# Optimization experiments

Measured on AMD Instinct MI355X. Metric: run time of the kernel, lower is better.

The kernel has to match this reference:

```python
import jax, jax.numpy as jnp
import numpy as np

DIM = 1024
HEADS = 8
DIM_HEAD = 64
INNER = HEADS * DIM_HEAD  # 512


def setup_inputs() -> dict:
    key = jax.random.key(0)
    k1, k2, k3, k4 = jax.random.split(key, 4)
    x = jax.random.normal(k1, (4, 4096, DIM), dtype=jnp.float32)
    W_qkv = jax.random.normal(k2, (DIM, 3 * INNER), dtype=jnp.float32) * (DIM ** -0.5)
    W_out = jax.random.normal(k3, (INNER, DIM), dtype=jnp.float32) * (INNER ** -0.5)
    b_out = jax.random.normal(k4, (DIM,), dtype=jnp.float32) * 0.01
    return {"x": x, "W_qkv": W_qkv, "W_out": W_out, "b_out": b_out}


def reference(x, W_qkv, W_out, b_out):
    b, n, _ = x.shape
    qkv = x @ W_qkv                                   # [b, n, 3*inner]
    q, k, v = jnp.split(qkv, 3, axis=-1)              # each [b, n, inner]

    def to_heads(t):
        return t.reshape(b, n, HEADS, DIM_HEAD).transpose(0, 2, 1, 3)  # [b, h, n, d]

    q = jax.nn.elu(to_heads(q)) + 1.0
    k = jax.nn.elu(to_heads(k)) + 1.0
    v = to_heads(v)
    # kv summary matrix: [b, h, d, e]
    context = jnp.einsum('bhnd,bhne->bhde', k, v)
    out = jnp.einsum('bhde,bhnd->bhne', context, q)   # [b, h, n, e]
    out = out.transpose(0, 2, 1, 3).reshape(b, n, INNER)
    return out @ W_out + b_out
```

## Files before the change

kernel.cpp:

```cpp
#include <hip/hip_runtime.h>
#include <hip/hip_bf16.h>
#include <cstdint>

typedef __attribute__((ext_vector_type(4))) float f32x4;
typedef __attribute__((ext_vector_type(8))) short bf16x8;

__device__ __forceinline__ ushort f2bf(float f) {
  unsigned u = __builtin_bit_cast(unsigned, f);
  u += 0x7fffu + ((u >> 16) & 1u);
  return (ushort)(u >> 16);
}

__device__ __forceinline__ void gload_lds16(const ushort* g, ushort* l) {
  __builtin_amdgcn_global_load_lds(
      (const __attribute__((address_space(1))) unsigned int*)g,
      (__attribute__((address_space(3))) unsigned int*)l, 16, 0, 0);
}

__device__ __forceinline__ void hard_barrier() {
  __builtin_amdgcn_sched_barrier(0);
  __builtin_amdgcn_s_barrier();
  __builtin_amdgcn_sched_barrier(0);
}

template <int N>
__device__ __forceinline__ void wait_vm() {
  if constexpr (N == 0) asm volatile("s_waitcnt vmcnt(0)" ::: "memory");
  else if constexpr (N == 2) asm volatile("s_waitcnt vmcnt(2)" ::: "memory");
  else if constexpr (N == 3) asm volatile("s_waitcnt vmcnt(3)" ::: "memory");
  else if constexpr (N == 4) asm volatile("s_waitcnt vmcnt(4)" ::: "memory");
  else static_assert(N < 0, "unsupported vmcnt");
}

__device__ __forceinline__ float elu1(float v) {
  return (v > 0.f) ? (v + 1.f) : __expf(v);
}

__global__ __launch_bounds__(256) void prep_kernel(const float4* __restrict__ x,
                                                   ushort4* __restrict__ xb,
                                                   const float* __restrict__ W,
                                                   ushort* __restrict__ Wt) {
  if (blockIdx.x < 2048) {
    const int n4 = 16384 * 1024 / 4;
    const int stride = 2048 * 256;
    for (int i = blockIdx.x * 256 + threadIdx.x; i < n4; i += stride) {
      float4 f = x[i];
      ushort4 o;
      o.x = f2bf(f.x); o.y = f2bf(f.y); o.z = f2bf(f.z); o.w = f2bf(f.w);
      xb[i] = o;
    }
  } else {
    __shared__ float tile[32][33];
    const int tb = blockIdx.x - 2048;
    const int n0 = (tb % 48) * 32;
    const int k0 = (tb / 48) * 32;
    const int tx = threadIdx.x & 31;
    const int ty = threadIdx.x >> 5;
    #pragma unroll
    for (int p = 0; p < 4; ++p) {
      int k = k0 + ty + p * 8;
      tile[ty + p * 8][tx] = W[(size_t)k * 1536 + n0 + tx];
    }
    __syncthreads();
    #pragma unroll
    for (int p = 0; p < 4; ++p) {
      int n = n0 + ty + p * 8;
      Wt[(size_t)n * 1024 + k0 + tx] = f2bf(tile[tx][ty + p * 8]);
    }
  }
}

template <int LDA, int LDB, int NT>
__device__ __forceinline__ void gemm_core32(const ushort* __restrict__ A,
                                            const ushort* __restrict__ Bt,
                                            int row0, int col0, f32x4 acc[4][4],
                                            ushort* lds) {
  const int tid = threadIdx.x;
  const int l = tid & 63;
  const int wid = tid >> 6;
  const int fr = l & 15;
  const int fq = l >> 4;
  const int wr = wid >> 2;
  const int wc = wid & 3;

  const int sc = ((tid & 3) ^ ((tid >> 3) & 3)) * 8;
  const ushort* aS = A + (size_t)(row0 + (tid >> 2)) * LDA + sc;
  const ushort* bS = Bt + (size_t)(col0 + (tid >> 2)) * LDB + sc;

  auto stage = [&](int t) {
    ushort* base = lds + (t % 3) * 12288 + tid * 8;
    gload_lds16(aS + t * 32, base);
    gload_lds16(bS + t * 32, base + 4096);
    gload_lds16(bS + (size_t)128 * LDB + t * 32, base + 8192);
  };

  const int sig = fq ^ ((fr >> 1) & 3);
  const int aOff = wr * 2048 + fr * 32 + sig * 8;
  const int bOff = 4096 + wc * 2048 + fr * 32 + sig * 8;

  auto compute = [&](int t) {
    const ushort* sb = lds + (t % 3) * 12288;
    bf16x8 av[4], bv[4];
    #pragma unroll
    for (int m = 0; m < 4; ++m) av[m] = *(const bf16x8*)(sb + aOff + m * 512);
    #pragma unroll
    for (int n = 0; n < 4; ++n) bv[n] = *(const bf16x8*)(sb + bOff + n * 512);
    __builtin_amdgcn_s_setprio(1);
    #pragma unroll
    for (int m = 0; m < 4; ++m)
      #pragma unroll
      for (int n = 0; n < 4; ++n)
        acc[m][n] = __builtin_amdgcn_mfma_f32_16x16x32_bf16(av[m], bv[n], acc[m][n], 0, 0, 0);
    __builtin_amdgcn_s_setprio(0);
  };

  stage(0);
  stage(1);
  wait_vm<3>();
  hard_barrier();

  #pragma unroll 3
  for (int t = 0; t < NT; ++t) {
    if (t + 2 < NT) stage(t + 2);
    compute(t);
    if (t + 2 < NT) {
      wait_vm<3>();
      hard_barrier();
    } else if (t + 1 < NT) {
      wait_vm<0>();
      hard_barrier();
    }
  }
}

__global__ __launch_bounds__(512, 4) void gemm_qkv_kernel(const ushort* __restrict__ xb,
                                                          const ushort* __restrict__ wt,
                                                          ushort* __restrict__ q,
                                                          ushort* __restrict__ kT,
                                                          ushort* __restrict__ vT) {
  __shared__ ushort lds[36864];
  f32x4 acc[4][4] = {};
  const int row0 = blockIdx.x * 128;
  const int col0 = blockIdx.y * 256;
  gemm_core32<1024, 1024, 32>(xb, wt, row0, col0, acc, lds);
  const int l = threadIdx.x & 63;
  const int wid = threadIdx.x >> 6;
  const int wr = wid >> 2, wc = wid & 3;
  const int fr = l & 15, fq = l >> 4;
  #pragma unroll
  for (int m = 0; m < 4; ++m) {
    #pragma unroll
    for (int n = 0; n < 4; ++n) {
      const int c = col0 + wc * 64 + n * 16 + fr;
      const int r0 = row0 + wr * 64 + m * 16 + fq * 4;
      if (c < 512) {
        #pragma unroll
        for (int j = 0; j < 4; ++j)
          q[(size_t)(r0 + j) * 512 + c] = f2bf(elu1(acc[m][n][j]));
      } else if (c < 1024) {
        const int d = c - 512;
        const int bh = (r0 >> 12) * 8 + (d >> 6);
        const int nn = r0 & 4095;
        ushort4 o;
        o.x = f2bf(elu1(acc[m][n][0]));
        o.y = f2bf(elu1(acc[m][n][1]));
        o.z = f2bf(elu1(acc[m][n][2]));
        o.w = f2bf(elu1(acc[m][n][3]));
        *(ushort4*)&kT[((size_t)bh * 64 + (d & 63)) * 4096 + nn] = o;
      } else {
        const int d = c - 1024;
        const int bh = (r0 >> 12) * 8 + (d >> 6);
        const int nn = r0 & 4095;
        ushort4 o;
        o.x = f2bf(acc[m][n][0]);
        o.y = f2bf(acc[m][n][1]);
        o.z = f2bf(acc[m][n][2]);
        o.w = f2bf(acc[m][n][3]);
        *(ushort4*)&vT[((size_t)bh * 64 + (d & 63)) * 4096 + nn] = o;
      }
    }
  }
}

__global__ __launch_bounds__(256) void ctx_mfma_kernel(const ushort* __restrict__ kT,
                                                       const ushort* __restrict__ vT,
                                                       float* __restrict__ part) {
  __shared__ ushort lds[16384];
  const int bh = blockIdx.x;
  const int sp = blockIdx.y;
  const int tid = threadIdx.x;
  const int l = tid & 63, wid = tid >> 6;
  const int fr = l & 15, fq = l >> 4;
  const int wr = wid >> 1, wc = wid & 1;

  const size_t base = (size_t)bh * 64 * 4096 + sp * 512;
  const int srow = tid >> 2;
  const int lam = (tid & 3) ^ ((tid >> 3) & 3);
  const ushort* aG = kT + base + (size_t)srow * 4096 + lam * 8;
  const ushort* bG = vT + base + (size_t)srow * 4096 + lam * 8;

  auto stage = [&](int t) {
    ushort* d = lds + (t & 3) * 4096 + tid * 8;
    gload_lds16(aG + t * 32, d);
    gload_lds16(bG + t * 32, d + 2048);
  };

  const int sig = fq ^ ((fr >> 1) & 3);
  f32x4 acc[2][2] = {};

  auto compute = [&](int t) {
    const ushort* sb = lds + (t & 3) * 4096;
    bf16x8 av[2], bv[2];
    #pragma unroll
    for (int mm = 0; mm < 2; ++mm)
      av[mm] = *(const bf16x8*)&sb[(wr * 32 + mm * 16 + fr) * 32 + sig * 8];
    #pragma unroll
    for (int nn = 0; nn < 2; ++nn)
      bv[nn] = *(const bf16x8*)&sb[2048 + (wc * 32 + nn * 16 + fr) * 32 + sig * 8];
    #pragma unroll
    for (int mm = 0; mm < 2; ++mm)
      #pragma unroll
      for (int nn = 0; nn < 2; ++nn)
        acc[mm][nn] = __builtin_amdgcn_mfma_f32_16x16x32_bf16(av[mm], bv[nn], acc[mm][nn], 0, 0, 0);
  };

  constexpr int NT = 16;
  stage(0); stage(1); stage(2);
  for (int t = 0; t < NT; ++t) {
    if (t <= NT - 3) wait_vm<4>();
    else if (t == NT - 2) wait_vm<2>();
    else wait_vm<0>();
    hard_barrier();
    compute(t);
    hard_barrier();
    if (t + 3 < NT) stage(t + 3);
  }

  float* dst = part + ((size_t)sp * 32 + bh) * 4096;
  #pragma unroll
  for (int mm = 0; mm < 2; ++mm)
    #pragma unroll
    for (int nn = 0; nn < 2; ++nn)
      #pragma unroll
      for (int j = 0; j < 4; ++j)
        dst[(wr * 32 + mm * 16 + fq * 4 + j) * 64 + wc * 32 + nn * 16 + fr] = acc[mm][nn][j];
}

__global__ __launch_bounds__(256) void weff_kernel(const float* __restrict__ part,
                                                   const float* __restrict__ Wout,
                                                   ushort* __restrict__ weff) {
  const int bh = blockIdx.x;
  const int h = bh & 7;
  const int m0 = blockIdx.y * 128;
  const int t = threadIdx.x;
  __shared__ float cs[64 * 64];
  __shared__ float ws[64][128];
  #pragma unroll
  for (int p = 0; p < 4; ++p) {
    const int idx = p * 1024 + t * 4;
    f32x4 s = {};
    #pragma unroll
    for (int sp = 0; sp < 8; ++sp)
      s += *(const f32x4*)&part[(size_t)sp * 131072 + (size_t)bh * 4096 + idx];
    *(f32x4*)&cs[idx] = s;
  }
  #pragma unroll
  for (int p = 0; p < 8; ++p) {
    const int e = (t >> 5) + p * 8;
    const int c = (t & 31) * 4;
    *(float4*)&ws[e][c] = *(const float4*)&Wout[(size_t)(h * 64 + e) * 1024 + m0 + c];
  }
  __syncthreads();
  const int m = t & 127;
  const int dh = (t >> 7) * 32;
  float acc[32] = {};
  for (int e = 0; e < 64; ++e) {
    const float w = ws[e][m];
    #pragma unroll
    for (int i = 0; i < 32; ++i)
      acc[i] += cs[(dh + i) * 64 + e] * w;
  }
  ushort* dst = weff + ((size_t)(bh >> 3) * 1024 + m0 + m) * 512 + h * 64 + dh;
  #pragma unroll
  for (int i = 0; i < 32; ++i) dst[i] = f2bf(acc[i]);
}

__global__ __launch_bounds__(512, 4) void gemm_out_kernel(const ushort* __restrict__ q,
                                                          const ushort* __restrict__ weff,
                                                          const float* __restrict__ bout,
                                                          float* __restrict__ out) {
  __shared__ ushort lds[36864];
  f32x4 acc[4][4] = {};
  const int row0 = blockIdx.x * 128;
  const int col0 = blockIdx.y * 256;
  const int b = row0 >> 12;
  gemm_core32<512, 512, 16>(q, weff + (size_t)b * 1024 * 512, row0, col0, acc, lds);
  const int l = threadIdx.x & 63;
  const int wid = threadIdx.x >> 6;
  const int wr = wid >> 2, wc = wid & 3;
  const int fr = l & 15, fq = l >> 4;
  #pragma unroll
  for (int m = 0; m < 4; ++m) {
    #pragma unroll
    for (int n = 0; n < 4; ++n) {
      const int c = col0 + wc * 64 + n * 16 + fr;
      const float bb = bout[c];
      #pragma unroll
      for (int j = 0; j < 4; ++j) {
        const int r = row0 + wr * 64 + m * 16 + fq * 4 + j;
        out[(size_t)r * 1024 + c] = acc[m][n][j] + bb;
      }
    }
  }
}

extern "C" void kernel_launch(void* const* d_in, const int* in_sizes, int n_in,
                              void* d_out, int out_size, void* d_ws, size_t ws_size,
                              hipStream_t stream) {
  const float* x    = (const float*)d_in[0];
  const float* Wqkv = (const float*)d_in[1];
  const float* Wout = (const float*)d_in[2];
  const float* bout = (const float*)d_in[3];
  float* out = (float*)d_out;
  char* ws = (char*)d_ws;

  ushort* xb   = (ushort*)(ws);
  float*  part = (float* )(ws);
  ushort* wt   = (ushort*)(ws + 33554432);
  ushort* q    = (ushort*)(ws + 36700160);
  ushort* kT   = (ushort*)(ws + 53477376);
  ushort* vT   = (ushort*)(ws + 70254592);
  ushort* weff = (ushort*)(ws + 87556096);

  prep_kernel<<<3584, 256, 0, stream>>>((const float4*)x, (ushort4*)xb, Wqkv, wt);
  gemm_qkv_kernel<<<dim3(128, 6), 512, 0, stream>>>(xb, wt, q, kT, vT);
  ctx_mfma_kernel<<<dim3(32, 8), 256, 0, stream>>>(kT, vT, part);
  weff_kernel<<<dim3(32, 8), 256, 0, stream>>>(part, Wout, weff);
  gemm_out_kernel<<<dim3(128, 4), 512, 0, stream>>>(q, weff, bout, out);
}
```

Baseline: 127.9 us.

## Use 256x128 tiles with 4 waves and 128-row warp tiles in QKV GEMM

Replaces the QKV projection GEMM core with a variant that uses 256 threads per block, each wave computing a 128x64 sub-tile (8x4 MFMA fragments) on a 256x128 block tile. The block tile has the same area as before, but each wave now does more MFMAs per LDS fragment load, which raises register-level reuse and cuts LDS read traffic. The launch grid changes to 64x12 blocks, the staging pattern and vmcnt wait depth are adjusted, and s_setprio is placed around the MFMA bursts. In exchange there is higher register pressure (128 accumulator registers), and fewer waves per block may give less latency hiding.

```diff
diff --git a/kernel.cpp b/kernel.cpp
--- a/kernel.cpp
+++ b/kernel.cpp
@@ -29,6 +29,7 @@
   else if constexpr (N == 2) asm volatile("s_waitcnt vmcnt(2)" ::: "memory");
   else if constexpr (N == 3) asm volatile("s_waitcnt vmcnt(3)" ::: "memory");
   else if constexpr (N == 4) asm volatile("s_waitcnt vmcnt(4)" ::: "memory");
+  else if constexpr (N == 6) asm volatile("s_waitcnt vmcnt(6)" ::: "memory");
   else static_assert(N < 0, "unsupported vmcnt");
 }
 
@@ -133,26 +134,98 @@
   }
 }
 
-__global__ __launch_bounds__(512, 4) void gemm_qkv_kernel(const ushort* __restrict__ xb,
+template <int LDA, int LDB, int NT>
+__device__ __forceinline__ void gemm_core_hr(const ushort* __restrict__ A,
+                                             const ushort* __restrict__ Bt,
+                                             int row0, int col0, f32x4 acc[8][4],
+                                             ushort* lds) {
+  const int tid = threadIdx.x;
+  const int l = tid & 63;
+  const int wid = tid >> 6;
+  const int fr = l & 15;
+  const int fq = l >> 4;
+  const int wr = wid >> 1;
+  const int wc = wid & 1;
+
+  const int sc = ((tid & 3) ^ ((tid >> 3) & 3)) * 8;
+  const ushort* aS = A + (size_t)(row0 + (tid >> 2)) * LDA + sc;
+  const ushort* bS = Bt + (size_t)(col0 + (tid >> 2)) * LDB + sc;
+
+  auto stage = [&](int t) {
+    ushort* base = lds + (t % 3) * 12288 + tid * 8;
+    #pragma unroll
+    for (int p = 0; p < 4; ++p)
+      gload_lds16(aS + (size_t)(p * 64) * LDA + t * 32, base + p * 2048);
+    #pragma unroll
+    for (int p = 0; p < 2; ++p)
+      gload_lds16(bS + (size_t)(p * 64) * LDB + t * 32, base + 8192 + p * 2048);
+  };
+
+  const int sig = fq ^ ((fr >> 1) & 3);
+  const int aOff = wr * 4096 + fr * 32 + sig * 8;
+  const int bOff = 8192 + wc * 2048 + fr * 32 + sig * 8;
+
+  auto compute = [&](int t) {
+    const ushort* sb = lds + (t % 3) * 12288;
+    bf16x8 bv[4];
+    #pragma unroll
+    for (int n = 0; n < 4; ++n) bv[n] = *(const bf16x8*)(sb + bOff + n * 512);
+    #pragma unroll
+    for (int mh = 0; mh < 2; ++mh) {
+      bf16x8 av[4];
+      #pragma unroll
+      for (int mm = 0; mm < 4; ++mm)
+        av[mm] = *(const bf16x8*)(sb + aOff + (mh * 4 + mm) * 512);
+      __builtin_amdgcn_s_setprio(1);
+      #pragma unroll
+      for (int mm = 0; mm < 4; ++mm)
+        #pragma unroll
+        for (int n = 0; n < 4; ++n)
+          acc[mh * 4 + mm][n] =
+              __builtin_amdgcn_mfma_f32_16x16x32_bf16(av[mm], bv[n], acc[mh * 4 + mm][n], 0, 0, 0);
+      __builtin_amdgcn_s_setprio(0);
+    }
+  };
+
+  stage(0);
+  stage(1);
+  wait_vm<6>();
+  hard_barrier();
+
+  #pragma unroll 3
+  for (int t = 0; t < NT; ++t) {
+    if (t + 2 < NT) stage(t + 2);
+    compute(t);
+    if (t + 2 < NT) {
+      wait_vm<6>();
+      hard_barrier();
+    } else if (t + 1 < NT) {
+      wait_vm<0>();
+      hard_barrier();
+    }
+  }
+}
+
+__global__ __launch_bounds__(256, 2) void gemm_qkv_kernel(const ushort* __restrict__ xb,
                                                           const ushort* __restrict__ wt,
                                                           ushort* __restrict__ q,
                                                           ushort* __restrict__ kT,
                                                           ushort* __restrict__ vT) {
   __shared__ ushort lds[36864];
-  f32x4 acc[4][4] = {};
-  const int row0 = blockIdx.x * 128;
-  const int col0 = blockIdx.y * 256;
-  gemm_core32<1024, 1024, 32>(xb, wt, row0, col0, acc, lds);
+  f32x4 acc[8][4] = {};
+  const int row0 = blockIdx.x * 256;
+  const int col0 = blockIdx.y * 128;
+  gemm_core_hr<1024, 1024, 32>(xb, wt, row0, col0, acc, lds);
   const int l = threadIdx.x & 63;
   const int wid = threadIdx.x >> 6;
-  const int wr = wid >> 2, wc = wid & 3;
+  const int wr = wid >> 1, wc = wid & 1;
   const int fr = l & 15, fq = l >> 4;
   #pragma unroll
-  for (int m = 0; m < 4; ++m) {
+  for (int m = 0; m < 8; ++m) {
     #pragma unroll
     for (int n = 0; n < 4; ++n) {
       const int c = col0 + wc * 64 + n * 16 + fr;
-      const int r0 = row0 + wr * 64 + m * 16 + fq * 4;
+      const int r0 = row0 + wr * 128 + m * 16 + fq * 4;
       if (c < 512) {
         #pragma unroll
         for (int j = 0; j < 4; ++j)
@@ -333,7 +406,7 @@
   ushort* weff = (ushort*)(ws + 87556096);
 
   prep_kernel<<<3584, 256, 0, stream>>>((const float4*)x, (ushort4*)xb, Wqkv, wt);
-  gemm_qkv_kernel<<<dim3(128, 6), 512, 0, stream>>>(xb, wt, q, kT, vT);
+  gemm_qkv_kernel<<<dim3(64, 12), 256, 0, stream>>>(xb, wt, q, kT, vT);
   ctx_mfma_kernel<<<dim3(32, 8), 256, 0, stream>>>(kT, vT, part);
   weff_kernel<<<dim3(32, 8), 256, 0, stream>>>(part, Wout, weff);
   gemm_out_kernel<<<dim3(128, 4), 512, 0, stream>>>(q, weff, bout, out);
```

Result: no change. 129.6 us (+1.4%).
